# Kernel tuning notes

Measured on AMD Instinct MI355X. Metric: run time of the kernel, lower is better.

## Reference

```python
import jax, jax.numpy as jnp
import numpy as np

C_S, C_Z, C_H = 384, 128, 32
N, L = 4, 384
EPS = 1e-5  # torch LayerNorm default


def setup_inputs() -> dict:
    key = jax.random.key(0)
    ks = jax.random.split(key, 8)
    s = jax.random.normal(ks[0], (N, L, C_S), dtype=jnp.float32)
    ln_g = jnp.ones((C_S,), jnp.float32)
    ln_b = jnp.zeros((C_S,), jnp.float32)
    W1 = jax.random.normal(ks[1], (C_S, C_H), jnp.float32) / np.sqrt(C_S)
    b1 = jax.random.normal(ks[2], (C_H,), jnp.float32) * 0.02
    W2 = jax.random.normal(ks[3], (C_S, C_H), jnp.float32) / np.sqrt(C_S)
    b2 = jax.random.normal(ks[4], (C_H,), jnp.float32) * 0.02
    # linear_out has init='final' (zeros) in training; use random values for a
    # meaningful numerical baseline.
    Wo = jax.random.normal(ks[5], (C_H * C_H, C_Z), jnp.float32) / np.sqrt(C_H * C_H)
    bo = jax.random.normal(ks[6], (C_Z,), jnp.float32) * 0.02
    return {"s": s, "ln_g": ln_g, "ln_b": ln_b, "W1": W1, "b1": b1,
            "W2": W2, "b2": b2, "Wo": Wo, "bo": bo}


def reference(s, ln_g, ln_b, W1, b1, W2, b2, Wo, bo):
    # LayerNorm over c_s
    mu = jnp.mean(s, axis=-1, keepdims=True)
    var = jnp.mean(jnp.square(s - mu), axis=-1, keepdims=True)
    sn = (s - mu) * jax.lax.rsqrt(var + EPS) * ln_g + ln_b
    a = sn @ W1 + b1  # [N, L, c_h]
    b = sn @ W2 + b2  # [N, L, c_h]
    # Original: outer product a[n,i,c]*b[n,j,d] flattened as c*c_h+d, then linear_out.
    # Algebraically fused: never materialize the [N,L,L,c_h^2] tensor.
    Wo3 = Wo.reshape(C_H, C_H, C_Z)  # index order (c, d, z) matches c*c_h+d flattening
    z = jnp.einsum('nic,njd,cdz->nijz', a, b, Wo3, optimize=True) + bo
    return z  # [N, L, L, c_z]
```

## Files before the change

kernel.cpp:

```cpp
#include <hip/hip_runtime.h>
#include <hip/hip_bf16.h>

#define CS 384
#define CH 32
#define CZ 128
#define LL 384
#define NL 1536
#define EPS 1e-5f

typedef float v4f __attribute__((ext_vector_type(4)));
typedef short s8v __attribute__((ext_vector_type(8)));
typedef unsigned short u8s __attribute__((ext_vector_type(8)));

static __device__ __forceinline__ unsigned short f2bf(float x) {
    unsigned int b = __float_as_uint(x);
    b += 0x7FFFu + ((b >> 16) & 1u);
    return (unsigned short)(b >> 16);
}

__global__ __launch_bounds__(256, 2) void k_prep(
    const float* __restrict__ s, const float* __restrict__ g, const float* __restrict__ be,
    const float* __restrict__ W1, const float* __restrict__ pb1,
    const float* __restrict__ W2, const float* __restrict__ pb2,
    const float* __restrict__ Wo,
    unsigned short* __restrict__ Bf, unsigned short* __restrict__ Mf)
{
    const int blk = blockIdx.x;
    const int r0  = blk * 4;
    const int t   = threadIdx.x;

    __shared__ float sn[4][392];
    __shared__ float Afl[4][CH];
    __shared__ __align__(16) float Msub[4 * 32 * 128];

    {
        const int w = t >> 6, lane = t & 63;
        const float* srow = s + (size_t)(r0 + w) * CS;
        float x[6];
        #pragma unroll
        for (int k = 0; k < 6; ++k) x[k] = srow[lane + k * 64];
        float p = x[0] + x[1] + x[2] + x[3] + x[4] + x[5];
        #pragma unroll
        for (int m = 1; m < 64; m <<= 1) p += __shfl_xor(p, m);
        const float mu = p * (1.0f / CS);
        float q = 0.f;
        #pragma unroll
        for (int k = 0; k < 6; ++k) { float d = x[k] - mu; q += d * d; }
        #pragma unroll
        for (int m = 1; m < 64; m <<= 1) q += __shfl_xor(q, m);
        const float rstd = rsqrtf(q * (1.0f / CS) + EPS);
        #pragma unroll
        for (int k = 0; k < 6; ++k) {
            const int c = lane + k * 64;
            sn[w][c] = (x[k] - mu) * rstd * g[c] + be[c];
        }
    }
    __syncthreads();

    {
        const int h = t & 31, mat = (t >> 5) & 1, rw = t >> 6;
        const float* W = mat ? W2 : W1;
        const float* snr = sn[rw];
        float acc = 0.f;
        #pragma unroll 8
        for (int c = 0; c < CS; ++c)
            acc += snr[c] * W[c * CH + h];
        acc += mat ? pb2[h] : pb1[h];
        if (!mat) {
            Afl[rw][h] = acc;
        } else {
            const int row = r0 + rw;
            const int n = row / LL, jr = row % LL;
            const int jt = jr >> 4, l16 = jr & 15;
            Bf[(((size_t)(n * 24 + jt)) * 64 + l16 + 16 * (h >> 3)) * 8 + (h & 7)] = f2bf(acc);
        }
    }
    __syncthreads();

    const v4f* Wo4 = (const v4f*)Wo;
    #pragma unroll
    for (int it = 0; it < 4; ++it) {
        const int col = t + it * 256;
        v4f acc[4];
        #pragma unroll
        for (int r = 0; r < 4; ++r) acc[r] = (v4f)(0.f);
        #pragma unroll 8
        for (int c = 0; c < CH; ++c) {
            const v4f wv = Wo4[(size_t)c * 1024 + col];
            #pragma unroll
            for (int r = 0; r < 4; ++r)
                acc[r] += Afl[r][c] * wv;
        }
        #pragma unroll
        for (int r = 0; r < 4; ++r)
            *((v4f*)&Msub[r * 4096 + col * 4]) = acc[r];
    }
    __syncthreads();

    #pragma unroll
    for (int i = 0; i < 8; ++i) {
        const int item = t + i * 256;
        const int l  = item & 63;
        const int zt = (item >> 6) & 7;
        const int rr = item >> 9;
        const int gq = l >> 4;
        const int z  = zt * 16 + (l & 15);
        u8s o;
        #pragma unroll
        for (int e = 0; e < 8; ++e)
            o[e] = f2bf(Msub[rr * 4096 + (gq * 8 + e) * 128 + z]);
        *(u8s*)(Mf + (((size_t)(r0 + rr) * 8 + zt) * 64 + l) * 8) = o;
    }
}

__global__ __launch_bounds__(256, 3) void k_out(
    const unsigned short* __restrict__ Bf, const unsigned short* __restrict__ Mf,
    const float* __restrict__ bo, float* __restrict__ out)
{
    const int r = blockIdx.x;
    const int t = threadIdx.x;
    const int l = t & 63, w = t >> 6;
    const int g = l >> 4, c16 = l & 15;
    const int li = l & 31, hi2 = l >> 5;
    const int n = r / LL;

    __shared__ __align__(16) float lds[4][2048];

    s8v mf[8];
    {
        const s8v* Mfr = (const s8v*)(Mf + (size_t)r * 8 * 64 * 8);
        #pragma unroll
        for (int zt = 0; zt < 8; ++zt) mf[zt] = Mfr[zt * 64 + l];
    }
    s8v af[6];
    {
        const s8v* Bfn = (const s8v*)(Bf + (size_t)n * 24 * 64 * 8);
        #pragma unroll
        for (int i = 0; i < 6; ++i) af[i] = Bfn[(w + i * 4) * 64 + l];
    }
    v4f bov[8];
    #pragma unroll
    for (int zt = 0; zt < 8; ++zt) bov[zt] = *(const v4f*)(bo + zt * 16 + g * 4);

    char* myl = (char*)lds[w];
    v4f* outv = (v4f*)(out + (size_t)r * LL * CZ);

    #pragma unroll
    for (int i = 0; i < 6; ++i) {
        const int jt = w + i * 4;

        #pragma unroll
        for (int zt = 0; zt < 8; ++zt) {
            v4f d = __builtin_amdgcn_mfma_f32_16x16x32_bf16(mf[zt], af[i], (v4f)(0.f), 0, 0, 0);
            d += bov[zt];
            const int byte = (c16 << 9) + (((zt << 6) + (g << 4)) ^ ((c16 & 7) << 4));
            *(v4f*)(myl + byte) = d;
        }
        asm volatile("s_waitcnt lgkmcnt(0)" ::: "memory");

        #pragma unroll
        for (int i2 = 0; i2 < 8; ++i2) {
            const int rr = 2 * i2 + hi2;
            const int byte = (rr << 9) + (((li << 4)) ^ ((rr & 7) << 4));
            const v4f v = *(const v4f*)(myl + byte);
            outv[(size_t)(jt * 16 + rr) * 32 + li] = v;
        }
    }
}

extern "C" void kernel_launch(void* const* d_in, const int* in_sizes, int n_in,
                              void* d_out, int out_size, void* d_ws, size_t ws_size,
                              hipStream_t stream) {
    const float* s  = (const float*)d_in[0];
    const float* g  = (const float*)d_in[1];
    const float* be = (const float*)d_in[2];
    const float* W1 = (const float*)d_in[3];
    const float* b1 = (const float*)d_in[4];
    const float* W2 = (const float*)d_in[5];
    const float* b2 = (const float*)d_in[6];
    const float* Wo = (const float*)d_in[7];
    const float* bo = (const float*)d_in[8];
    float* out = (float*)d_out;

    if (ws_size < 98304u + 12582912u) return;
    unsigned short* Bf = (unsigned short*)d_ws;
    unsigned short* Mf = (unsigned short*)((char*)d_ws + 98304);

    k_prep<<<NL / 4, 256, 0, stream>>>(s, g, be, W1, b1, W2, b2, Wo, Bf, Mf);
    k_out <<<NL, 256, 0, stream>>>(Bf, Mf, bo, out);
}
```

Measured before the change: 85.64 us.

## Split k_prep across four z-quarter blocks per row group with bf16 LDS staging

```diff
diff --git a/kernel.cpp b/kernel.cpp
--- a/kernel.cpp
+++ b/kernel.cpp
@@ -18,7 +18,7 @@
     return (unsigned short)(b >> 16);
 }
 
-__global__ __launch_bounds__(256, 2) void k_prep(
+__global__ __launch_bounds__(256, 4) void k_prep(
     const float* __restrict__ s, const float* __restrict__ g, const float* __restrict__ be,
     const float* __restrict__ W1, const float* __restrict__ pb1,
     const float* __restrict__ W2, const float* __restrict__ pb2,
@@ -26,12 +26,14 @@
     unsigned short* __restrict__ Bf, unsigned short* __restrict__ Mf)
 {
     const int blk = blockIdx.x;
-    const int r0  = blk * 4;
+    const int rg  = blk >> 2;
+    const int qz  = blk & 3;
+    const int r0  = rg * 4;
     const int t   = threadIdx.x;
 
     __shared__ float sn[4][392];
     __shared__ float Afl[4][CH];
-    __shared__ __align__(16) float Msub[4 * 32 * 128];
+    __shared__ __align__(8) unsigned short MsubS[4 * 32 * 36];
 
     {
         const int w = t >> 6, lane = t & 63;
@@ -59,16 +61,20 @@
 
     {
         const int h = t & 31, mat = (t >> 5) & 1, rw = t >> 6;
-        const float* W = mat ? W2 : W1;
-        const float* snr = sn[rw];
-        float acc = 0.f;
-        #pragma unroll 8
-        for (int c = 0; c < CS; ++c)
-            acc += snr[c] * W[c * CH + h];
-        acc += mat ? pb2[h] : pb1[h];
         if (!mat) {
-            Afl[rw][h] = acc;
-        } else {
+            const float* snr = sn[rw];
+            float acc = 0.f;
+            #pragma unroll 8
+            for (int c = 0; c < CS; ++c)
+                acc += snr[c] * W1[c * CH + h];
+            Afl[rw][h] = acc + pb1[h];
+        } else if (qz == 0) {
+            const float* snr = sn[rw];
+            float acc = 0.f;
+            #pragma unroll 8
+            for (int c = 0; c < CS; ++c)
+                acc += snr[c] * W2[c * CH + h];
+            acc += pb2[h];
             const int row = r0 + rw;
             const int n = row / LL, jr = row % LL;
             const int jt = jr >> 4, l16 = jr & 15;
@@ -77,10 +83,11 @@
     }
     __syncthreads();
 
-    const v4f* Wo4 = (const v4f*)Wo;
-    #pragma unroll
-    for (int it = 0; it < 4; ++it) {
-        const int col = t + it * 256;
+    {
+        const v4f* Wo4 = (const v4f*)Wo;
+        const int d   = t >> 3;
+        const int zq8 = t & 7;
+        const int col = d * 32 + (qz << 3) + zq8;
         v4f acc[4];
         #pragma unroll
         for (int r = 0; r < 4; ++r) acc[r] = (v4f)(0.f);
@@ -92,23 +99,28 @@
                 acc[r] += Afl[r][c] * wv;
         }
         #pragma unroll
-        for (int r = 0; r < 4; ++r)
-            *((v4f*)&Msub[r * 4096 + col * 4]) = acc[r];
+        for (int r = 0; r < 4; ++r) {
+            ushort4 hh;
+            hh.x = f2bf(acc[r].x); hh.y = f2bf(acc[r].y);
+            hh.z = f2bf(acc[r].z); hh.w = f2bf(acc[r].w);
+            *(ushort4*)&MsubS[(r * 32 + d) * 36 + zq8 * 4] = hh;
+        }
     }
     __syncthreads();
 
     #pragma unroll
-    for (int i = 0; i < 8; ++i) {
+    for (int i = 0; i < 2; ++i) {
         const int item = t + i * 256;
-        const int l  = item & 63;
-        const int zt = (item >> 6) & 7;
-        const int rr = item >> 9;
-        const int gq = l >> 4;
-        const int z  = zt * 16 + (l & 15);
+        const int l   = item & 63;
+        const int ztl = (item >> 6) & 1;
+        const int rr  = item >> 7;
+        const int zt  = (qz << 1) + ztl;
+        const int zloc = ztl * 16 + (l & 15);
+        const int gq  = l >> 4;
         u8s o;
         #pragma unroll
         for (int e = 0; e < 8; ++e)
-            o[e] = f2bf(Msub[rr * 4096 + (gq * 8 + e) * 128 + z]);
+            o[e] = MsubS[(rr * 32 + gq * 8 + e) * 36 + zloc];
         *(u8s*)(Mf + (((size_t)(r0 + rr) * 8 + zt) * 64 + l) * 8) = o;
     }
 }
@@ -186,6 +198,6 @@
     unsigned short* Bf = (unsigned short*)d_ws;
     unsigned short* Mf = (unsigned short*)((char*)d_ws + 98304);
 
-    k_prep<<<NL / 4, 256, 0, stream>>>(s, g, be, W1, b1, W2, b2, Wo, Bf, Mf);
+    k_prep<<<NL, 256, 0, stream>>>(s, g, be, W1, b1, W2, b2, Wo, Bf, Mf);
     k_out <<<NL, 256, 0, stream>>>(Bf, Mf, bo, out);
 }
```

Measured after the change: 100.9 us. 17.9% more time.

## Fuse per-row LayerNorm, A projection and M computation into output kernel

Applied to the files above, without the earlier changes.

```diff
diff --git a/kernel.cpp b/kernel.cpp
--- a/kernel.cpp
+++ b/kernel.cpp
@@ -18,20 +18,16 @@
     return (unsigned short)(b >> 16);
 }
 
-__global__ __launch_bounds__(256, 2) void k_prep(
+__global__ __launch_bounds__(256) void k_bf(
     const float* __restrict__ s, const float* __restrict__ g, const float* __restrict__ be,
-    const float* __restrict__ W1, const float* __restrict__ pb1,
     const float* __restrict__ W2, const float* __restrict__ pb2,
-    const float* __restrict__ Wo,
-    unsigned short* __restrict__ Bf, unsigned short* __restrict__ Mf)
+    unsigned short* __restrict__ BfG)
 {
-    const int blk = blockIdx.x;
-    const int r0  = blk * 4;
-    const int t   = threadIdx.x;
+    const int r0 = blockIdx.x * 4;
+    const int t  = threadIdx.x;
 
     __shared__ float sn[4][392];
-    __shared__ float Afl[4][CH];
-    __shared__ __align__(16) float Msub[4 * 32 * 128];
+    __shared__ float part[4][2][32];
 
     {
         const int w = t >> 6, lane = t & 63;
@@ -58,91 +54,124 @@
     __syncthreads();
 
     {
-        const int h = t & 31, mat = (t >> 5) & 1, rw = t >> 6;
-        const float* W = mat ? W2 : W1;
+        const int h = t & 31, ch = (t >> 5) & 1, rw = t >> 6;
         const float* snr = sn[rw];
         float acc = 0.f;
+        const int c0 = ch * 192;
         #pragma unroll 8
-        for (int c = 0; c < CS; ++c)
-            acc += snr[c] * W[c * CH + h];
-        acc += mat ? pb2[h] : pb1[h];
-        if (!mat) {
-            Afl[rw][h] = acc;
-        } else {
-            const int row = r0 + rw;
-            const int n = row / LL, jr = row % LL;
-            const int jt = jr >> 4, l16 = jr & 15;
-            Bf[(((size_t)(n * 24 + jt)) * 64 + l16 + 16 * (h >> 3)) * 8 + (h & 7)] = f2bf(acc);
-        }
-    }
-    __syncthreads();
-
-    const v4f* Wo4 = (const v4f*)Wo;
-    #pragma unroll
-    for (int it = 0; it < 4; ++it) {
-        const int col = t + it * 256;
-        v4f acc[4];
-        #pragma unroll
-        for (int r = 0; r < 4; ++r) acc[r] = (v4f)(0.f);
-        #pragma unroll 8
-        for (int c = 0; c < CH; ++c) {
-            const v4f wv = Wo4[(size_t)c * 1024 + col];
-            #pragma unroll
-            for (int r = 0; r < 4; ++r)
-                acc[r] += Afl[r][c] * wv;
-        }
-        #pragma unroll
-        for (int r = 0; r < 4; ++r)
-            *((v4f*)&Msub[r * 4096 + col * 4]) = acc[r];
-    }
-    __syncthreads();
-
-    #pragma unroll
-    for (int i = 0; i < 8; ++i) {
-        const int item = t + i * 256;
-        const int l  = item & 63;
-        const int zt = (item >> 6) & 7;
-        const int rr = item >> 9;
-        const int gq = l >> 4;
-        const int z  = zt * 16 + (l & 15);
-        u8s o;
-        #pragma unroll
-        for (int e = 0; e < 8; ++e)
-            o[e] = f2bf(Msub[rr * 4096 + (gq * 8 + e) * 128 + z]);
-        *(u8s*)(Mf + (((size_t)(r0 + rr) * 8 + zt) * 64 + l) * 8) = o;
-    }
-}
-
-__global__ __launch_bounds__(256, 3) void k_out(
-    const unsigned short* __restrict__ Bf, const unsigned short* __restrict__ Mf,
+        for (int c = c0; c < c0 + 192; ++c)
+            acc += snr[c] * W2[c * CH + h];
+        part[rw][ch][h] = acc;
+    }
+    __syncthreads();
+
+    if (t < 128) {
+        const int rw = t >> 5, h = t & 31;
+        const float v = part[rw][0][h] + part[rw][1][h] + pb2[h];
+        const int row = r0 + rw;
+        const int n = row / LL, jr = row % LL;
+        const int jt = jr >> 4, l16 = jr & 15;
+        BfG[(((size_t)(n * 24 + jt)) * 64 + l16 + 16 * (h >> 3)) * 8 + (h & 7)] = f2bf(v);
+    }
+}
+
+__global__ __launch_bounds__(256, 3) void k_out_f(
+    const float* __restrict__ s, const float* __restrict__ g, const float* __restrict__ be,
+    const float* __restrict__ W1, const float* __restrict__ pb1,
+    const float* __restrict__ Wo, const unsigned short* __restrict__ BfG,
     const float* __restrict__ bo, float* __restrict__ out)
 {
     const int r = blockIdx.x;
     const int t = threadIdx.x;
     const int l = t & 63, w = t >> 6;
-    const int g = l >> 4, c16 = l & 15;
+    const int g2 = l >> 4, c16 = l & 15;
     const int li = l & 31, hi2 = l >> 5;
     const int n = r / LL;
 
-    __shared__ __align__(16) float lds[4][2048];
+    __shared__ float sn[392];
+    __shared__ float red[8];
+    __shared__ float part[8][32];
+    __shared__ float Afl[CH];
+    __shared__ __align__(16) float Msub[4096];
+    __shared__ __align__(16) float bounce[4][2048];
+
+    {
+        const float* srow = s + (size_t)r * CS;
+        const float e0 = srow[t];
+        const float e1 = (t < 128) ? srow[256 + t] : 0.f;
+        float p = e0 + e1;
+        #pragma unroll
+        for (int m = 1; m < 64; m <<= 1) p += __shfl_xor(p, m);
+        if (l == 0) red[w] = p;
+        __syncthreads();
+        const float mu = (red[0] + red[1] + red[2] + red[3]) * (1.0f / CS);
+        __syncthreads();
+        const float d0 = e0 - mu, d1 = e1 - mu;
+        float q = d0 * d0 + ((t < 128) ? d1 * d1 : 0.f);
+        #pragma unroll
+        for (int m = 1; m < 64; m <<= 1) q += __shfl_xor(q, m);
+        if (l == 0) red[w] = q;
+        __syncthreads();
+        const float var = (red[0] + red[1] + red[2] + red[3]) * (1.0f / CS);
+        const float rstd = rsqrtf(var + EPS);
+        sn[t] = d0 * rstd * g[t] + be[t];
+        if (t < 128) sn[256 + t] = d1 * rstd * g[256 + t] + be[256 + t];
+    }
+    __syncthreads();
+
+    {
+        const int h = t & 31, cs = t >> 5;
+        float acc = 0.f;
+        const int c0 = cs * 48;
+        #pragma unroll 8
+        for (int c = c0; c < c0 + 48; ++c)
+            acc += sn[c] * W1[c * CH + h];
+        part[cs][h] = acc;
+    }
+    __syncthreads();
+    if (t < 32) {
+        float a = pb1[t];
+        #pragma unroll
+        for (int k = 0; k < 8; ++k) a += part[k][t];
+        Afl[t] = a;
+    }
+    __syncthreads();
+
+    {
+        const v4f* Wo4 = (const v4f*)Wo;
+        #pragma unroll
+        for (int it = 0; it < 4; ++it) {
+            const int col = t + it * 256;
+            v4f acc = (v4f)(0.f);
+            #pragma unroll 8
+            for (int c = 0; c < CH; ++c)
+                acc += Afl[c] * Wo4[(size_t)c * 1024 + col];
+            *(v4f*)&Msub[col * 4] = acc;
+        }
+    }
+    __syncthreads();
 
     s8v mf[8];
-    {
-        const s8v* Mfr = (const s8v*)(Mf + (size_t)r * 8 * 64 * 8);
-        #pragma unroll
-        for (int zt = 0; zt < 8; ++zt) mf[zt] = Mfr[zt * 64 + l];
-    }
+    #pragma unroll
+    for (int zt = 0; zt < 8; ++zt) {
+        u8s o;
+        #pragma unroll
+        for (int e = 0; e < 8; ++e)
+            o[e] = f2bf(Msub[(g2 * 8 + e) * 128 + zt * 16 + c16]);
+        mf[zt] = (s8v)o;
+    }
+
     s8v af[6];
     {
-        const s8v* Bfn = (const s8v*)(Bf + (size_t)n * 24 * 64 * 8);
+        const s8v* Bfn = (const s8v*)(BfG + (size_t)n * 24 * 64 * 8);
         #pragma unroll
         for (int i = 0; i < 6; ++i) af[i] = Bfn[(w + i * 4) * 64 + l];
     }
     v4f bov[8];
     #pragma unroll
-    for (int zt = 0; zt < 8; ++zt) bov[zt] = *(const v4f*)(bo + zt * 16 + g * 4);
-
-    char* myl = (char*)lds[w];
+    for (int zt = 0; zt < 8; ++zt) bov[zt] = *(const v4f*)(bo + zt * 16 + g2 * 4);
+
+    char* myl = (char*)bounce[w];
     v4f* outv = (v4f*)(out + (size_t)r * LL * CZ);
 
     #pragma unroll
@@ -153,17 +182,17 @@
         for (int zt = 0; zt < 8; ++zt) {
             v4f d = __builtin_amdgcn_mfma_f32_16x16x32_bf16(mf[zt], af[i], (v4f)(0.f), 0, 0, 0);
             d += bov[zt];
-            const int byte = (c16 << 9) + (((zt << 6) + (g << 4)) ^ ((c16 & 7) << 4));
+            const int byte = (c16 << 9) + (((zt << 6) + (g2 << 4)) ^ ((c16 & 7) << 4));
             *(v4f*)(myl + byte) = d;
         }
         asm volatile("s_waitcnt lgkmcnt(0)" ::: "memory");
 
         #pragma unroll
         for (int i2 = 0; i2 < 8; ++i2) {
-            const int rr = 2 * i2 + hi2;
-            const int byte = (rr << 9) + (((li << 4)) ^ ((rr & 7) << 4));
+            const int rw2 = 2 * i2 + hi2;
+            const int byte = (rw2 << 9) + (((li << 4)) ^ ((rw2 & 7) << 4));
             const v4f v = *(const v4f*)(myl + byte);
-            outv[(size_t)(jt * 16 + rr) * 32 + li] = v;
+            outv[(size_t)(jt * 16 + rw2) * 32 + li] = v;
         }
     }
 }
@@ -182,10 +211,9 @@
     const float* bo = (const float*)d_in[8];
     float* out = (float*)d_out;
 
-    if (ws_size < 98304u + 12582912u) return;
+    if (ws_size < 98304u) return;
     unsigned short* Bf = (unsigned short*)d_ws;
-    unsigned short* Mf = (unsigned short*)((char*)d_ws + 98304);
-
-    k_prep<<<NL / 4, 256, 0, stream>>>(s, g, be, W1, b1, W2, b2, Wo, Bf, Mf);
-    k_out <<<NL, 256, 0, stream>>>(Bf, Mf, bo, out);
-}
+
+    k_bf   <<<NL / 4, 256, 0, stream>>>(s, g, be, W2, b2, Bf);
+    k_out_f<<<NL, 256, 0, stream>>>(s, g, be, W1, b1, Wo, Bf, bo, out);
+}
```

New measurement: 85.55 us. About the same (-0.1%).
